# Kernel tuning notes

Measured on AMD Instinct MI355X. Metric: run time of the kernel, lower is better.

The kernel has to match this reference:

```python
import jax, jax.numpy as jnp
import numpy as np

N_NODES = 50000
N_EDGES = 600000
HIDDEN = 128
N_GRAPHS = 64


def _gcn_conv(x, src, dst, W, b):
    # PyG GCNConv: h = x @ W; add self-loops; sym-normalized scatter-add; + bias.
    h = x @ W  # [N, D]
    ones = jnp.ones((src.shape[0],), dtype=x.dtype)
    deg = jax.ops.segment_sum(ones, dst, num_segments=N_NODES) + 1.0  # self-loop
    dinv = jax.lax.rsqrt(deg)  # deg^{-1/2}
    norm = dinv[src] * dinv[dst]  # [E]
    agg = jax.ops.segment_sum(h[src] * norm[:, None], dst, num_segments=N_NODES)
    # self-loop contribution: deg[i]^{-1/2} * deg[i]^{-1/2} * h[i] = h[i] / deg[i]
    return agg + h * (1.0 / deg)[:, None] + b


def _sage_conv(x, src, dst, W_l, W_r, b):
    # PyG SAGEConv (mean aggr): out = mean_neigh(x) @ W_l + x @ W_r + b
    ones = jnp.ones((src.shape[0],), dtype=x.dtype)
    cnt = jax.ops.segment_sum(ones, dst, num_segments=N_NODES)
    s = jax.ops.segment_sum(x[src], dst, num_segments=N_NODES)
    mean = s / jnp.maximum(cnt, 1.0)[:, None]
    return mean @ W_l + x @ W_r + b


def setup_inputs() -> dict:
    key = jax.random.key(0)
    ks = jax.random.split(key, 12)
    sc = 1.0 / np.sqrt(HIDDEN)
    x = jax.random.normal(ks[0], (N_NODES, HIDDEN), dtype=jnp.float32)
    edge_index = jax.random.randint(ks[1], (2, N_EDGES), 0, N_NODES, dtype=jnp.int64)
    batch = jnp.sort(jax.random.randint(ks[2], (N_NODES,), 0, N_GRAPHS, dtype=jnp.int64))
    W1 = jax.random.uniform(ks[3], (HIDDEN, HIDDEN), jnp.float32, -sc, sc)
    b1 = jnp.zeros((HIDDEN,), jnp.float32)
    W2 = jax.random.uniform(ks[4], (HIDDEN, HIDDEN), jnp.float32, -sc, sc)
    b2 = jnp.zeros((HIDDEN,), jnp.float32)
    W_l = jax.random.uniform(ks[5], (HIDDEN, HIDDEN), jnp.float32, -sc, sc)
    W_r = jax.random.uniform(ks[6], (HIDDEN, HIDDEN), jnp.float32, -sc, sc)
    b_s = jnp.zeros((HIDDEN,), jnp.float32)
    return {"x": x, "edge_index": edge_index, "batch": batch,
            "W1": W1, "b1": b1, "W2": W2, "b2": b2,
            "W_l": W_l, "W_r": W_r, "b_s": b_s}


def reference(x, edge_index, batch, W1, b1, W2, b2, W_l, W_r, b_s):
    src, dst = edge_index[0], edge_index[1]
    h = jax.nn.relu(_gcn_conv(x, src, dst, W1, b1))
    h = jax.nn.relu(_gcn_conv(h, src, dst, W2, b2))
    h = _sage_conv(h, src, dst, W_l, W_r, b_s)
    # global_mean_pool over graph ids
    ones = jnp.ones((N_NODES,), dtype=h.dtype)
    cnt = jax.ops.segment_sum(ones, batch, num_segments=N_GRAPHS)
    s = jax.ops.segment_sum(h, batch, num_segments=N_GRAPHS)
    return s / jnp.maximum(cnt, 1.0)[:, None]
```

## Files before the change

kernel.cpp:

```cpp
#include <hip/hip_runtime.h>

#define N_NODES 50000
#define N_EDGES 600000
#define HIDDEN 128
#define N_GRAPHS 64
#define SLICES 16
#define SCAN_B ((N_NODES + 255) / 256)

typedef __attribute__((ext_vector_type(8))) short bf16x8;
typedef __attribute__((ext_vector_type(4))) float f32x4;

__device__ inline ushort f2bf(float v) {
    union { float f; unsigned u; } x; x.f = v;
    unsigned r = (x.u + 0x7FFF + ((x.u >> 16) & 1)) >> 16;
    return (ushort)r;
}
__device__ inline float bf2f(ushort h) {
    union { unsigned u; float f; } x; x.u = ((unsigned)h) << 16;
    return x.f;
}



__global__ void deg_kernel(const int* __restrict__ dst, int* __restrict__ deg) {
    int t = blockIdx.x * 256 + threadIdx.x;
    if (t < N_EDGES) atomicAdd(&deg[dst[t]], 1);
}


__global__ void scan_partial(const int* __restrict__ deg, int* __restrict__ bsum) {
    const int b = blockIdx.x, t = threadIdx.x;
    const int i = b * 256 + t;
    int v = (i < N_NODES) ? deg[i] : 0;
    __shared__ int wsum[4];
#pragma unroll
    for (int o = 32; o > 0; o >>= 1) v += __shfl_down(v, o, 64);
    if ((t & 63) == 0) wsum[t >> 6] = v;
    __syncthreads();
    if (t == 0) bsum[b] = wsum[0] + wsum[1] + wsum[2] + wsum[3];
}

__global__ void scan_bsum(const int* __restrict__ bsum, int* __restrict__ boff,
                          int* __restrict__ rowptr) {
    __shared__ int s[256];
    const int t = threadIdx.x;
    const int v = (t < SCAN_B) ? bsum[t] : 0;
    s[t] = v;
    __syncthreads();
    for (int o = 1; o < 256; o <<= 1) {
        int u = (t >= o) ? s[t - o] : 0;
        __syncthreads();
        s[t] += u;
        __syncthreads();
    }
    if (t < SCAN_B) boff[t] = s[t] - v;
    if (t == 255) rowptr[N_NODES] = s[255];
}

__global__ void scan_final(const int* __restrict__ deg, const int* __restrict__ boff,
                           int* __restrict__ rowptr, float* __restrict__ dinv) {
    const int b = blockIdx.x, t = threadIdx.x;
    const int i = b * 256 + t;
    __shared__ int s[256];
    const int v = (i < N_NODES) ? deg[i] : 0;
    s[t] = v;
    __syncthreads();
    for (int o = 1; o < 256; o <<= 1) {
        int u = (t >= o) ? s[t - o] : 0;
        __syncthreads();
        s[t] += u;
        __syncthreads();
    }
    if (i < N_NODES) {
        rowptr[i] = boff[b] + s[t] - v;
        dinv[i] = rsqrtf((float)v + 1.0f);
    }
}


__global__ void fill_kernel(const int* __restrict__ src, const int* __restrict__ dst,
                            const int* __restrict__ rowptr, int* __restrict__ fillcnt,
                            const float* __restrict__ dinv, int2* __restrict__ csr) {
    int e = blockIdx.x * 256 + threadIdx.x;
    if (e >= N_EDGES) return;
    const int d = dst[e];
    const int s = src[e];
    const int pos = rowptr[d] + atomicAdd(&fillcnt[d], 1);
    csr[pos] = make_int2(s, __float_as_int(dinv[s] * dinv[d]));
}


__global__ void pack_w(const float* __restrict__ Wa, const float* __restrict__ Wb,
                       const float* __restrict__ Wc, const float* __restrict__ Wd,
                       ushort* __restrict__ out) {
    const int m = blockIdx.x >> 3;
    const int gid = (blockIdx.x & 7) * 256 + threadIdx.x;
    const float* W = (m == 0) ? Wa : (m == 1) ? Wb : (m == 2) ? Wc : Wd;
    const int s = gid >> 9;
    const int c = (gid >> 6) & 7;
    const int lane = gid & 63;
    const int kbase = s * 32 + 8 * (lane >> 4);
    const int n = c * 16 + (lane & 15);
    ushort* hi = out + (long)m * 32768;
    ushort* lo = hi + 16384;
#pragma unroll
    for (int j = 0; j < 8; j++) {
        const float v = W[(kbase + j) * HIDDEN + n];
        const ushort h = f2bf(v);
        hi[gid * 8 + j] = h;
        lo[gid * 8 + j] = f2bf(v - bf2f(h));
    }
}


template <bool CHA>
__global__ void gemm_mfma(const float* __restrict__ A, const ushort* __restrict__ Wp,
                          ushort* __restrict__ Cb, int nrows) {
    __shared__ alignas(16) ushort Ah[64 * 128];
    __shared__ alignas(16) ushort Al[64 * 128];
    const int r0 = blockIdx.x * 64;
    const int tid = threadIdx.x;

#pragma unroll
    for (int i = 0; i < 8; i++) {
        const int idx = tid + i * 256;
        const int node = idx >> 5;
        float4 v = make_float4(0.f, 0.f, 0.f, 0.f);
        int f0;
        if (CHA) {
            const int c = (idx >> 2) & 7;
            const int f4 = idx & 3;
            f0 = c * 16 + f4 * 4;
            if (r0 + node < nrows)
                v = reinterpret_cast<const float4*>(A)[((long)c * N_NODES + r0 + node) * 4 + f4];
        } else {
            f0 = 4 * (idx & 31);
            if (r0 + node < nrows)
                v = reinterpret_cast<const float4*>(A + (long)r0 * HIDDEN)[idx];
        }
        const ushort h0 = f2bf(v.x), h1 = f2bf(v.y), h2 = f2bf(v.z), h3 = f2bf(v.w);
        ushort4 h4; h4.x = h0; h4.y = h1; h4.z = h2; h4.w = h3;
        ushort4 l4;
        l4.x = f2bf(v.x - bf2f(h0)); l4.y = f2bf(v.y - bf2f(h1));
        l4.z = f2bf(v.z - bf2f(h2)); l4.w = f2bf(v.w - bf2f(h3));
        const int kb = (2 * f0) ^ ((node & 7) << 4);
        *reinterpret_cast<ushort4*>(&Ah[(node * 256 + kb) >> 1]) = h4;
        *reinterpret_cast<ushort4*>(&Al[(node * 256 + kb) >> 1]) = l4;
    }
    __syncthreads();

    const int wave = tid >> 6;
    const int lane = tid & 63;
    const int arow = 16 * wave + (lane & 15);

    f32x4 acc[8];
#pragma unroll
    for (int c = 0; c < 8; c++) acc[c] = (f32x4){0.f, 0.f, 0.f, 0.f};

#pragma unroll
    for (int s = 0; s < 4; s++) {
        const int koff = (s * 64 + ((lane >> 4) << 4)) ^ ((arow & 7) << 4);
        const bf16x8 ahi = *reinterpret_cast<const bf16x8*>(&Ah[(arow * 256 + koff) >> 1]);
        const bf16x8 alo = *reinterpret_cast<const bf16x8*>(&Al[(arow * 256 + koff) >> 1]);
#pragma unroll
        for (int c = 0; c < 8; c++) {
            const bf16x8 bhi = *reinterpret_cast<const bf16x8*>(&Wp[((s * 8 + c) * 64 + lane) * 8]);
            const bf16x8 blo = *reinterpret_cast<const bf16x8*>(&Wp[16384 + ((s * 8 + c) * 64 + lane) * 8]);
            acc[c] = __builtin_amdgcn_mfma_f32_16x16x32_bf16(ahi, bhi, acc[c], 0, 0, 0);
            acc[c] = __builtin_amdgcn_mfma_f32_16x16x32_bf16(alo, bhi, acc[c], 0, 0, 0);
            acc[c] = __builtin_amdgcn_mfma_f32_16x16x32_bf16(ahi, blo, acc[c], 0, 0, 0);
        }
    }

    const int node0 = r0 + 16 * wave + ((lane >> 4) << 2);
    const int fc = lane & 15;
#pragma unroll
    for (int c = 0; c < 8; c++) {
#pragma unroll
        for (int reg = 0; reg < 4; reg++) {
            const int node = node0 + reg;
            if (node < nrows)
                Cb[(long)node * HIDDEN + c * 16 + fc] = f2bf(acc[c][reg]);
        }
    }
}


__global__ void gemm_sage_mfma(const float* __restrict__ A1, const ushort* __restrict__ Wp1,
                               const float* __restrict__ A2, const ushort* __restrict__ Wp2,
                               const float* __restrict__ bias, float* __restrict__ C,
                               int nrows) {
    __shared__ alignas(16) ushort Ah[64 * 128];
    __shared__ alignas(16) ushort Al[64 * 128];
    const int r0 = blockIdx.x * 64;
    const int tid = threadIdx.x;
    const int wave = tid >> 6;
    const int lane = tid & 63;
    const int arow = 16 * wave + (lane & 15);

    f32x4 acc[8];
#pragma unroll
    for (int c = 0; c < 8; c++) acc[c] = (f32x4){0.f, 0.f, 0.f, 0.f};

    for (int p = 0; p < 2; p++) {
        const float* A = (p == 0) ? A1 : A2;
        const ushort* Wp = (p == 0) ? Wp1 : Wp2;
        if (p) __syncthreads();
#pragma unroll
        for (int i = 0; i < 8; i++) {
            const int idx = tid + i * 256;
            const int node = idx >> 5;
            const int c = (idx >> 2) & 7;
            const int f4 = idx & 3;
            const int f0 = c * 16 + f4 * 4;
            float4 v = make_float4(0.f, 0.f, 0.f, 0.f);
            if (r0 + node < nrows)
                v = reinterpret_cast<const float4*>(A)[((long)c * N_NODES + r0 + node) * 4 + f4];
            const ushort h0 = f2bf(v.x), h1 = f2bf(v.y), h2 = f2bf(v.z), h3 = f2bf(v.w);
            ushort4 h4; h4.x = h0; h4.y = h1; h4.z = h2; h4.w = h3;
            ushort4 l4;
            l4.x = f2bf(v.x - bf2f(h0)); l4.y = f2bf(v.y - bf2f(h1));
            l4.z = f2bf(v.z - bf2f(h2)); l4.w = f2bf(v.w - bf2f(h3));
            const int kb = (2 * f0) ^ ((node & 7) << 4);
            *reinterpret_cast<ushort4*>(&Ah[(node * 256 + kb) >> 1]) = h4;
            *reinterpret_cast<ushort4*>(&Al[(node * 256 + kb) >> 1]) = l4;
        }
        __syncthreads();

#pragma unroll
        for (int s = 0; s < 4; s++) {
            const int koff = (s * 64 + ((lane >> 4) << 4)) ^ ((arow & 7) << 4);
            const bf16x8 ahi = *reinterpret_cast<const bf16x8*>(&Ah[(arow * 256 + koff) >> 1]);
            const bf16x8 alo = *reinterpret_cast<const bf16x8*>(&Al[(arow * 256 + koff) >> 1]);
#pragma unroll
            for (int c = 0; c < 8; c++) {
                const bf16x8 bhi = *reinterpret_cast<const bf16x8*>(&Wp[((s * 8 + c) * 64 + lane) * 8]);
                const bf16x8 blo = *reinterpret_cast<const bf16x8*>(&Wp[16384 + ((s * 8 + c) * 64 + lane) * 8]);
                acc[c] = __builtin_amdgcn_mfma_f32_16x16x32_bf16(ahi, bhi, acc[c], 0, 0, 0);
                acc[c] = __builtin_amdgcn_mfma_f32_16x16x32_bf16(alo, bhi, acc[c], 0, 0, 0);
                acc[c] = __builtin_amdgcn_mfma_f32_16x16x32_bf16(ahi, blo, acc[c], 0, 0, 0);
            }
        }
    }

    const int node0 = r0 + 16 * wave + ((lane >> 4) << 2);
    const int fc = lane & 15;
#pragma unroll
    for (int c = 0; c < 8; c++) {
        const float bb = bias[c * 16 + fc];
#pragma unroll
        for (int reg = 0; reg < 4; reg++) {
            const int node = node0 + reg;
            if (node < nrows)
                C[((long)c * N_NODES + node) * 16 + fc] = acc[c][reg] + bb;
        }
    }
}


template <bool WB16>
__global__ void gather_gcn(const ushort* __restrict__ hb, const int* __restrict__ rowptr,
                           const int2* __restrict__ csr, const float* __restrict__ dinv,
                           const float* __restrict__ bias, float* __restrict__ outC,
                           ushort* __restrict__ outB) {
    const int tid = threadIdx.x;
    const int d = blockIdx.x * 8 + (tid >> 5);
    if (d >= N_NODES) return;
    const int l = tid & 31;
    const float di = dinv[d];
    const int beg = rowptr[d];
    const int end = rowptr[d + 1];
    float a0 = 0.f, a1 = 0.f, a2 = 0.f, a3 = 0.f;
    int j = beg;
    for (; j + 2 <= end; j += 2) {
        const int2 e0 = csr[j];
        const int2 e1 = csr[j + 1];
        const float n0 = __int_as_float(e0.y);
        const float n1 = __int_as_float(e1.y);
        const ushort4 u0 = *reinterpret_cast<const ushort4*>(hb + (long)e0.x * HIDDEN + l * 4);
        const ushort4 u1 = *reinterpret_cast<const ushort4*>(hb + (long)e1.x * HIDDEN + l * 4);
        a0 += bf2f(u0.x) * n0 + bf2f(u1.x) * n1;
        a1 += bf2f(u0.y) * n0 + bf2f(u1.y) * n1;
        a2 += bf2f(u0.z) * n0 + bf2f(u1.z) * n1;
        a3 += bf2f(u0.w) * n0 + bf2f(u1.w) * n1;
    }
    if (j < end) {
        const int2 e0 = csr[j];
        const float n0 = __int_as_float(e0.y);
        const ushort4 u0 = *reinterpret_cast<const ushort4*>(hb + (long)e0.x * HIDDEN + l * 4);
        a0 += bf2f(u0.x) * n0;
        a1 += bf2f(u0.y) * n0;
        a2 += bf2f(u0.z) * n0;
        a3 += bf2f(u0.w) * n0;
    }
    const ushort4 us = *reinterpret_cast<const ushort4*>(hb + (long)d * HIDDEN + l * 4);
    const float4 b = *reinterpret_cast<const float4*>(bias + l * 4);
    const float invdeg = di * di;
    float4 res;
    res.x = fmaxf(a0 + bf2f(us.x) * invdeg + b.x, 0.f);
    res.y = fmaxf(a1 + bf2f(us.y) * invdeg + b.y, 0.f);
    res.z = fmaxf(a2 + bf2f(us.z) * invdeg + b.z, 0.f);
    res.w = fmaxf(a3 + bf2f(us.w) * invdeg + b.w, 0.f);
    *reinterpret_cast<float4*>(outC + ((long)(l >> 2) * N_NODES + d) * 16 + (l & 3) * 4) = res;
    if (WB16) {
        ushort4 o;
        o.x = f2bf(res.x); o.y = f2bf(res.y); o.z = f2bf(res.z); o.w = f2bf(res.w);
        *reinterpret_cast<ushort4*>(outB + (long)d * HIDDEN + l * 4) = o;
    }
}


__global__ void gather_sage(const ushort* __restrict__ hb, const int* __restrict__ rowptr,
                            const int2* __restrict__ csr, float* __restrict__ mean) {
    const int tid = threadIdx.x;
    const int d = blockIdx.x * 8 + (tid >> 5);
    if (d >= N_NODES) return;
    const int l = tid & 31;
    const int beg = rowptr[d];
    const int end = rowptr[d + 1];
    float a0 = 0.f, a1 = 0.f, a2 = 0.f, a3 = 0.f;
    int j = beg;
    for (; j + 2 <= end; j += 2) {
        const int2 e0 = csr[j];
        const int2 e1 = csr[j + 1];
        const ushort4 u0 = *reinterpret_cast<const ushort4*>(hb + (long)e0.x * HIDDEN + l * 4);
        const ushort4 u1 = *reinterpret_cast<const ushort4*>(hb + (long)e1.x * HIDDEN + l * 4);
        a0 += bf2f(u0.x) + bf2f(u1.x);
        a1 += bf2f(u0.y) + bf2f(u1.y);
        a2 += bf2f(u0.z) + bf2f(u1.z);
        a3 += bf2f(u0.w) + bf2f(u1.w);
    }
    if (j < end) {
        const int2 e0 = csr[j];
        const ushort4 u0 = *reinterpret_cast<const ushort4*>(hb + (long)e0.x * HIDDEN + l * 4);
        a0 += bf2f(u0.x);
        a1 += bf2f(u0.y);
        a2 += bf2f(u0.z);
        a3 += bf2f(u0.w);
    }
    const float inv = 1.0f / fmaxf((float)(end - beg), 1.0f);
    float4 res;
    res.x = a0 * inv; res.y = a1 * inv; res.z = a2 * inv; res.w = a3 * inv;
    *reinterpret_cast<float4*>(mean + ((long)(l >> 2) * N_NODES + d) * 16 + (l & 3) * 4) = res;
}


__device__ int lower_bound_batch(const int* __restrict__ batch, int key) {
    int lo = 0, hi = N_NODES;
    while (lo < hi) {
        int mid = (lo + hi) >> 1;
        if (batch[mid] < key) lo = mid + 1;
        else hi = mid;
    }
    return lo;
}

__global__ void pool_partial(const float* __restrict__ node, const int* __restrict__ batch,
                             float* __restrict__ part) {
    const int b = blockIdx.x;
    const int g = b / SLICES;
    const int k = b % SLICES;
    const int t = threadIdx.x;
    const long cbase = (long)(t >> 4) * N_NODES;
    const int foff = t & 15;
    const int lo = lower_bound_batch(batch, g);
    const int hi = lower_bound_batch(batch, g + 1);
    const int len = hi - lo;
    const int per = (len + SLICES - 1) / SLICES;
    const int s = lo + k * per;
    const int e = min(s + per, hi);
    float acc = 0.f;
    for (int i = s; i < e; i++) acc += node[(cbase + i) * 16 + foff];
    part[(long)b * HIDDEN + t] = acc;
}

__global__ void pool_reduce(const float* __restrict__ part, const int* __restrict__ batch,
                            float* __restrict__ out) {
    const int g = blockIdx.x;
    const int t = threadIdx.x;
    float acc = 0.f;
#pragma unroll
    for (int k = 0; k < SLICES; k++) acc += part[(long)(g * SLICES + k) * HIDDEN + t];
    const int lo = lower_bound_batch(batch, g);
    const int hi = lower_bound_batch(batch, g + 1);
    out[g * HIDDEN + t] = acc / fmaxf((float)(hi - lo), 1.0f);
}


extern "C" void kernel_launch(void* const* d_in, const int* in_sizes, int n_in,
                              void* d_out, int out_size, void* d_ws, size_t ws_size,
                              hipStream_t stream) {
    const float* x    = (const float*)d_in[0];
    const int*   ei   = (const int*)d_in[1];
    const int*   batch= (const int*)d_in[2];
    const float* W1   = (const float*)d_in[3];
    const float* b1   = (const float*)d_in[4];
    const float* W2   = (const float*)d_in[5];
    const float* b2   = (const float*)d_in[6];
    const float* W_l  = (const float*)d_in[7];
    const float* W_r  = (const float*)d_in[8];
    const float* b_s  = (const float*)d_in[9];
    float* out = (float*)d_out;

    const int* src = ei;
    const int* dst = ei + N_EDGES;

    char* ws = (char*)d_ws;
    const size_t NB = (size_t)N_NODES * HIDDEN * sizeof(float);
    float* B1 = (float*)(ws);
    float* B2 = (float*)(ws + NB);
    float* B3 = (float*)(ws + 2 * NB);
    ushort* HB1 = (ushort*)B2;
    ushort* HB2 = (ushort*)B1;
    size_t off = 3 * NB;
    int*   deg      = (int*)(ws + off);   off += (size_t)N_NODES * 4;
    float* dinv     = (float*)(ws + off); off += (size_t)N_NODES * 4;
    int*   rowptr   = (int*)(ws + off);   off += (size_t)(N_NODES + 1) * 4;
    int*   fillcnt  = (int*)(ws + off);   off += (size_t)N_NODES * 4;
    int2*  csr      = (int2*)(ws + off);  off += (size_t)N_EDGES * 8;
    float* part     = (float*)(ws + off); off += (size_t)N_GRAPHS * SLICES * HIDDEN * 4;
    int*   bsum     = (int*)(ws + off);   off += (size_t)SCAN_B * 4;
    int*   boff     = (int*)(ws + off);   off += (size_t)SCAN_B * 4;
    ushort* wpack   = (ushort*)(ws + off); off += (size_t)4 * 32768 * 2;

    const ushort* Wp1 = wpack;
    const ushort* Wp2 = wpack + 32768;
    const ushort* WpL = wpack + 2 * 32768;
    const ushort* WpR = wpack + 3 * 32768;

    const int EB = (N_EDGES + 255) / 256;
    const int GB = (N_NODES + 63) / 64;
    const int GTB = (N_NODES + 7) / 8;

    pack_w<<<32, 256, 0, stream>>>(W1, W2, W_l, W_r, wpack);

    hipMemsetAsync(deg, 0, (size_t)N_NODES * 4, stream);
    hipMemsetAsync(fillcnt, 0, (size_t)N_NODES * 4, stream);
    deg_kernel<<<EB, 256, 0, stream>>>(dst, deg);
    scan_partial<<<SCAN_B, 256, 0, stream>>>(deg, bsum);
    scan_bsum<<<1, 256, 0, stream>>>(bsum, boff, rowptr);
    scan_final<<<SCAN_B, 256, 0, stream>>>(deg, boff, rowptr, dinv);
    fill_kernel<<<EB, 256, 0, stream>>>(src, dst, rowptr, fillcnt, dinv, csr);

    gemm_mfma<false><<<GB, 256, 0, stream>>>(x, Wp1, HB1, N_NODES);
    gather_gcn<false><<<GTB, 256, 0, stream>>>(HB1, rowptr, csr, dinv, b1, B1, nullptr);

    gemm_mfma<true><<<GB, 256, 0, stream>>>(B1, Wp2, HB1, N_NODES);
    gather_gcn<true><<<GTB, 256, 0, stream>>>(HB1, rowptr, csr, dinv, b2, B3, HB2);

    gather_sage<<<GTB, 256, 0, stream>>>(HB2, rowptr, csr, B2);
    gemm_sage_mfma<<<GB, 256, 0, stream>>>(B2, WpL, B3, WpR, b_s, B1, N_NODES);

    pool_partial<<<N_GRAPHS * SLICES, 128, 0, stream>>>(B1, batch, part);
    pool_reduce<<<N_GRAPHS, 128, 0, stream>>>(part, batch, out);
}
```

Baseline: 269.6 us.

## Store intermediate activations in bf16 and drop low-part MFMA passes

Gather kernels now write their layer outputs as bf16 in row-major layout instead of fp32 in a chunked layout. The second GCN GEMM and the SAGE GEMM stage those bf16 rows straight into shared memory, skipping the hi/lo split and one of three MFMAs per step. This cuts global memory traffic for intermediate buffers, shared memory usage and MFMA count. The cost is lower precision for activations, which are now rounded to bf16 between layers.

Measured after the change: 260.2 us. 3.5% less time.

```diff
diff --git a/kernel.cpp b/kernel.cpp
--- a/kernel.cpp
+++ b/kernel.cpp
@@ -113,9 +113,8 @@
 }
 
 
-template <bool CHA>
-__global__ void gemm_mfma(const float* __restrict__ A, const ushort* __restrict__ Wp,
-                          ushort* __restrict__ Cb, int nrows) {
+__global__ void gemm_f32in(const float* __restrict__ A, const ushort* __restrict__ Wp,
+                           ushort* __restrict__ Cb, int nrows) {
     __shared__ alignas(16) ushort Ah[64 * 128];
     __shared__ alignas(16) ushort Al[64 * 128];
     const int r0 = blockIdx.x * 64;
@@ -125,19 +124,10 @@
     for (int i = 0; i < 8; i++) {
         const int idx = tid + i * 256;
         const int node = idx >> 5;
+        const int f0 = 4 * (idx & 31);
         float4 v = make_float4(0.f, 0.f, 0.f, 0.f);
-        int f0;
-        if (CHA) {
-            const int c = (idx >> 2) & 7;
-            const int f4 = idx & 3;
-            f0 = c * 16 + f4 * 4;
-            if (r0 + node < nrows)
-                v = reinterpret_cast<const float4*>(A)[((long)c * N_NODES + r0 + node) * 4 + f4];
-        } else {
-            f0 = 4 * (idx & 31);
-            if (r0 + node < nrows)
-                v = reinterpret_cast<const float4*>(A + (long)r0 * HIDDEN)[idx];
-        }
+        if (r0 + node < nrows)
+            v = reinterpret_cast<const float4*>(A + (long)r0 * HIDDEN)[idx];
         const ushort h0 = f2bf(v.x), h1 = f2bf(v.y), h2 = f2bf(v.z), h3 = f2bf(v.w);
         ushort4 h4; h4.x = h0; h4.y = h1; h4.z = h2; h4.w = h3;
         ushort4 l4;
@@ -186,12 +176,71 @@
 }
 
 
-__global__ void gemm_sage_mfma(const float* __restrict__ A1, const ushort* __restrict__ Wp1,
-                               const float* __restrict__ A2, const ushort* __restrict__ Wp2,
-                               const float* __restrict__ bias, float* __restrict__ C,
-                               int nrows) {
+__device__ inline void stage_bf16(const ushort* __restrict__ Ab, ushort* __restrict__ Ah,
+                                  int r0, int tid, int nrows) {
+#pragma unroll
+    for (int i = 0; i < 4; i++) {
+        const int idx = tid + i * 256;
+        const int node = idx >> 4;
+        const int g = idx & 15;
+        bf16x8 v = (bf16x8){0, 0, 0, 0, 0, 0, 0, 0};
+        if (r0 + node < nrows)
+            v = *reinterpret_cast<const bf16x8*>(Ab + (long)(r0 + node) * HIDDEN + g * 8);
+        const int kb = (g * 16) ^ ((node & 7) << 4);
+        *reinterpret_cast<bf16x8*>(&Ah[(node * 256 + kb) >> 1]) = v;
+    }
+}
+
+
+__global__ void gemm_bf16in(const ushort* __restrict__ Ab, const ushort* __restrict__ Wp,
+                            ushort* __restrict__ Cb, int nrows) {
     __shared__ alignas(16) ushort Ah[64 * 128];
-    __shared__ alignas(16) ushort Al[64 * 128];
+    const int r0 = blockIdx.x * 64;
+    const int tid = threadIdx.x;
+
+    stage_bf16(Ab, Ah, r0, tid, nrows);
+    __syncthreads();
+
+    const int wave = tid >> 6;
+    const int lane = tid & 63;
+    const int arow = 16 * wave + (lane & 15);
+
+    f32x4 acc[8];
+#pragma unroll
+    for (int c = 0; c < 8; c++) acc[c] = (f32x4){0.f, 0.f, 0.f, 0.f};
+
+#pragma unroll
+    for (int s = 0; s < 4; s++) {
+        const int koff = (s * 64 + ((lane >> 4) << 4)) ^ ((arow & 7) << 4);
+        const bf16x8 ahi = *reinterpret_cast<const bf16x8*>(&Ah[(arow * 256 + koff) >> 1]);
+#pragma unroll
+        for (int c = 0; c < 8; c++) {
+            const bf16x8 bhi = *reinterpret_cast<const bf16x8*>(&Wp[((s * 8 + c) * 64 + lane) * 8]);
+            const bf16x8 blo = *reinterpret_cast<const bf16x8*>(&Wp[16384 + ((s * 8 + c) * 64 + lane) * 8]);
+            acc[c] = __builtin_amdgcn_mfma_f32_16x16x32_bf16(ahi, bhi, acc[c], 0, 0, 0);
+            acc[c] = __builtin_amdgcn_mfma_f32_16x16x32_bf16(ahi, blo, acc[c], 0, 0, 0);
+        }
+    }
+
+    const int node0 = r0 + 16 * wave + ((lane >> 4) << 2);
+    const int fc = lane & 15;
+#pragma unroll
+    for (int c = 0; c < 8; c++) {
+#pragma unroll
+        for (int reg = 0; reg < 4; reg++) {
+            const int node = node0 + reg;
+            if (node < nrows)
+                Cb[(long)node * HIDDEN + c * 16 + fc] = f2bf(acc[c][reg]);
+        }
+    }
+}
+
+
+__global__ void gemm_sage_bf16in(const ushort* __restrict__ A1, const ushort* __restrict__ Wp1,
+                                 const ushort* __restrict__ A2, const ushort* __restrict__ Wp2,
+                                 const float* __restrict__ bias, float* __restrict__ C,
+                                 int nrows) {
+    __shared__ alignas(16) ushort Ah[64 * 128];
     const int r0 = blockIdx.x * 64;
     const int tid = threadIdx.x;
     const int wave = tid >> 6;
@@ -203,41 +252,21 @@
     for (int c = 0; c < 8; c++) acc[c] = (f32x4){0.f, 0.f, 0.f, 0.f};
 
     for (int p = 0; p < 2; p++) {
-        const float* A = (p == 0) ? A1 : A2;
+        const ushort* Ab = (p == 0) ? A1 : A2;
         const ushort* Wp = (p == 0) ? Wp1 : Wp2;
         if (p) __syncthreads();
-#pragma unroll
-        for (int i = 0; i < 8; i++) {
-            const int idx = tid + i * 256;
-            const int node = idx >> 5;
-            const int c = (idx >> 2) & 7;
-            const int f4 = idx & 3;
-            const int f0 = c * 16 + f4 * 4;
-            float4 v = make_float4(0.f, 0.f, 0.f, 0.f);
-            if (r0 + node < nrows)
-                v = reinterpret_cast<const float4*>(A)[((long)c * N_NODES + r0 + node) * 4 + f4];
-            const ushort h0 = f2bf(v.x), h1 = f2bf(v.y), h2 = f2bf(v.z), h3 = f2bf(v.w);
-            ushort4 h4; h4.x = h0; h4.y = h1; h4.z = h2; h4.w = h3;
-            ushort4 l4;
-            l4.x = f2bf(v.x - bf2f(h0)); l4.y = f2bf(v.y - bf2f(h1));
-            l4.z = f2bf(v.z - bf2f(h2)); l4.w = f2bf(v.w - bf2f(h3));
-            const int kb = (2 * f0) ^ ((node & 7) << 4);
-            *reinterpret_cast<ushort4*>(&Ah[(node * 256 + kb) >> 1]) = h4;
-            *reinterpret_cast<ushort4*>(&Al[(node * 256 + kb) >> 1]) = l4;
-        }
+        stage_bf16(Ab, Ah, r0, tid, nrows);
         __syncthreads();
 
 #pragma unroll
         for (int s = 0; s < 4; s++) {
             const int koff = (s * 64 + ((lane >> 4) << 4)) ^ ((arow & 7) << 4);
             const bf16x8 ahi = *reinterpret_cast<const bf16x8*>(&Ah[(arow * 256 + koff) >> 1]);
-            const bf16x8 alo = *reinterpret_cast<const bf16x8*>(&Al[(arow * 256 + koff) >> 1]);
 #pragma unroll
             for (int c = 0; c < 8; c++) {
                 const bf16x8 bhi = *reinterpret_cast<const bf16x8*>(&Wp[((s * 8 + c) * 64 + lane) * 8]);
                 const bf16x8 blo = *reinterpret_cast<const bf16x8*>(&Wp[16384 + ((s * 8 + c) * 64 + lane) * 8]);
                 acc[c] = __builtin_amdgcn_mfma_f32_16x16x32_bf16(ahi, bhi, acc[c], 0, 0, 0);
-                acc[c] = __builtin_amdgcn_mfma_f32_16x16x32_bf16(alo, bhi, acc[c], 0, 0, 0);
                 acc[c] = __builtin_amdgcn_mfma_f32_16x16x32_bf16(ahi, blo, acc[c], 0, 0, 0);
             }
         }
@@ -258,11 +287,9 @@
 }
 
 
-template <bool WB16>
 __global__ void gather_gcn(const ushort* __restrict__ hb, const int* __restrict__ rowptr,
                            const int2* __restrict__ csr, const float* __restrict__ dinv,
-                           const float* __restrict__ bias, float* __restrict__ outC,
-                           ushort* __restrict__ outB) {
+                           const float* __restrict__ bias, ushort* __restrict__ outB) {
     const int tid = threadIdx.x;
     const int d = blockIdx.x * 8 + (tid >> 5);
     if (d >= N_NODES) return;
@@ -296,22 +323,17 @@
     const ushort4 us = *reinterpret_cast<const ushort4*>(hb + (long)d * HIDDEN + l * 4);
     const float4 b = *reinterpret_cast<const float4*>(bias + l * 4);
     const float invdeg = di * di;
-    float4 res;
-    res.x = fmaxf(a0 + bf2f(us.x) * invdeg + b.x, 0.f);
-    res.y = fmaxf(a1 + bf2f(us.y) * invdeg + b.y, 0.f);
-    res.z = fmaxf(a2 + bf2f(us.z) * invdeg + b.z, 0.f);
-    res.w = fmaxf(a3 + bf2f(us.w) * invdeg + b.w, 0.f);
-    *reinterpret_cast<float4*>(outC + ((long)(l >> 2) * N_NODES + d) * 16 + (l & 3) * 4) = res;
-    if (WB16) {
-        ushort4 o;
-        o.x = f2bf(res.x); o.y = f2bf(res.y); o.z = f2bf(res.z); o.w = f2bf(res.w);
-        *reinterpret_cast<ushort4*>(outB + (long)d * HIDDEN + l * 4) = o;
-    }
+    ushort4 o;
+    o.x = f2bf(fmaxf(a0 + bf2f(us.x) * invdeg + b.x, 0.f));
+    o.y = f2bf(fmaxf(a1 + bf2f(us.y) * invdeg + b.y, 0.f));
+    o.z = f2bf(fmaxf(a2 + bf2f(us.z) * invdeg + b.z, 0.f));
+    o.w = f2bf(fmaxf(a3 + bf2f(us.w) * invdeg + b.w, 0.f));
+    *reinterpret_cast<ushort4*>(outB + (long)d * HIDDEN + l * 4) = o;
 }
 
 
 __global__ void gather_sage(const ushort* __restrict__ hb, const int* __restrict__ rowptr,
-                            const int2* __restrict__ csr, float* __restrict__ mean) {
+                            const int2* __restrict__ csr, ushort* __restrict__ mean) {
     const int tid = threadIdx.x;
     const int d = blockIdx.x * 8 + (tid >> 5);
     if (d >= N_NODES) return;
@@ -339,9 +361,10 @@
         a3 += bf2f(u0.w);
     }
     const float inv = 1.0f / fmaxf((float)(end - beg), 1.0f);
-    float4 res;
-    res.x = a0 * inv; res.y = a1 * inv; res.z = a2 * inv; res.w = a3 * inv;
-    *reinterpret_cast<float4*>(mean + ((long)(l >> 2) * N_NODES + d) * 16 + (l & 3) * 4) = res;
+    ushort4 o;
+    o.x = f2bf(a0 * inv); o.y = f2bf(a1 * inv);
+    o.z = f2bf(a2 * inv); o.w = f2bf(a3 * inv);
+    *reinterpret_cast<ushort4*>(mean + (long)d * HIDDEN + l * 4) = o;
 }
 
 
@@ -407,11 +430,12 @@
 
     char* ws = (char*)d_ws;
     const size_t NB = (size_t)N_NODES * HIDDEN * sizeof(float);
-    float* B1 = (float*)(ws);
-    float* B2 = (float*)(ws + NB);
-    float* B3 = (float*)(ws + 2 * NB);
-    ushort* HB1 = (ushort*)B2;
-    ushort* HB2 = (ushort*)B1;
+    const size_t HB = (size_t)N_NODES * HIDDEN * sizeof(ushort);
+    float*  SOUT = (float*)(ws);
+    ushort* HP   = (ushort*)(ws + NB);
+    ushort* G1   = (ushort*)(ws + NB + HB);
+    ushort* G2   = (ushort*)(ws + 2 * NB);
+    ushort* MEAN = (ushort*)(ws + 2 * NB + HB);
     size_t off = 3 * NB;
     int*   deg      = (int*)(ws + off);   off += (size_t)N_NODES * 4;
     float* dinv     = (float*)(ws + off); off += (size_t)N_NODES * 4;
@@ -442,15 +466,15 @@
     scan_final<<<SCAN_B, 256, 0, stream>>>(deg, boff, rowptr, dinv);
     fill_kernel<<<EB, 256, 0, stream>>>(src, dst, rowptr, fillcnt, dinv, csr);
 
-    gemm_mfma<false><<<GB, 256, 0, stream>>>(x, Wp1, HB1, N_NODES);
-    gather_gcn<false><<<GTB, 256, 0, stream>>>(HB1, rowptr, csr, dinv, b1, B1, nullptr);
-
-    gemm_mfma<true><<<GB, 256, 0, stream>>>(B1, Wp2, HB1, N_NODES);
-    gather_gcn<true><<<GTB, 256, 0, stream>>>(HB1, rowptr, csr, dinv, b2, B3, HB2);
-
-    gather_sage<<<GTB, 256, 0, stream>>>(HB2, rowptr, csr, B2);
-    gemm_sage_mfma<<<GB, 256, 0, stream>>>(B2, WpL, B3, WpR, b_s, B1, N_NODES);
-
-    pool_partial<<<N_GRAPHS * SLICES, 128, 0, stream>>>(B1, batch, part);
+    gemm_f32in<<<GB, 256, 0, stream>>>(x, Wp1, HP, N_NODES);
+    gather_gcn<<<GTB, 256, 0, stream>>>(HP, rowptr, csr, dinv, b1, G1);
+
+    gemm_bf16in<<<GB, 256, 0, stream>>>(G1, Wp2, HP, N_NODES);
+    gather_gcn<<<GTB, 256, 0, stream>>>(HP, rowptr, csr, dinv, b2, G2);
+
+    gather_sage<<<GTB, 256, 0, stream>>>(G2, rowptr, csr, MEAN);
+    gemm_sage_bf16in<<<GB, 256, 0, stream>>>(MEAN, WpL, G2, WpR, b_s, SOUT, N_NODES);
+
+    pool_partial<<<N_GRAPHS * SLICES, 128, 0, stream>>>(SOUT, batch, part);
     pool_reduce<<<N_GRAPHS, 128, 0, stream>>>(part, batch, out);
 }
```
